# Kernel optimization log

Hardware: AMD Instinct MI355X
Metric: run time of the kernel (lower is better)

## Reference

```python
import jax, jax.numpy as jnp
import numpy as np

B = 8192          # batch
DEPTH = 2         # variational layers
NCLS = 10         # classes
WIRES = 4         # qubits -> 16-dim statevector
NPATCH = 196      # 14x14 patches of 2x2 on a 28x28 image

# Pauli-Z expectation table: row i = (+1/-1) per wire for basis state i (wire 0 = MSB)
_bits = (np.arange(16)[:, None] >> np.array([3, 2, 1, 0])) & 1
_ZTAB = jnp.asarray(1.0 - 2.0 * _bits, dtype=jnp.float32)  # (16, 4)


def _ry(state, ang, wire):
    # Apply RY(ang) (real rotation) on `wire`; state shape (N,2,2,2,2)
    c = jnp.cos(0.5 * ang)
    s = jnp.sin(0.5 * ang)
    a0 = jnp.take(state, 0, axis=wire + 1)
    a1 = jnp.take(state, 1, axis=wire + 1)
    return jnp.stack([c * a0 - s * a1, s * a0 + c * a1], axis=wire + 1)


def _cnot01(state):  # control wire 0 (axis 1), target wire 1 (axis 2)
    return jnp.stack([state[:, 0], state[:, 1, ::-1]], axis=1)


def _cnot23(state):  # control wire 2 (axis 3), target wire 3 (axis 4)
    return jnp.stack([state[:, :, :, 0], state[:, :, :, 1, ::-1]], axis=3)


def _quanv(patches, theta):
    # patches: (N, 4) pixel angles. Batched 4-qubit statevector simulation.
    half = 0.5 * patches
    v = jnp.stack([jnp.cos(half), jnp.sin(half)], axis=-1)  # (N,4,2): RY(x_w)|0>
    state = jnp.einsum('na,nb,nc,nd->nabcd', v[:, 0], v[:, 1], v[:, 2], v[:, 3])
    for d in range(theta.shape[0]):
        for w in range(WIRES):
            state = _ry(state, theta[d, w], w)
        state = _cnot01(state)
        state = _cnot23(state)
    probs = (state * state).reshape(state.shape[0], 16)
    return probs @ _ZTAB  # (N, 4) <Z_w> expectations


def setup_inputs() -> dict:
    key = jax.random.key(0)
    k1, k2, k3 = jax.random.split(key, 3)
    x = jax.random.normal(k1, (B, 1, 28, 28), dtype=jnp.float32)
    theta = jax.random.normal(k2, (DEPTH, WIRES), dtype=jnp.float32)
    W = jax.random.normal(k3, (NCLS, NPATCH * WIRES), dtype=jnp.float32) * 0.03
    b = jnp.zeros((NCLS,), dtype=jnp.float32)
    return {"x": x, "theta": theta, "W": W, "b": b}


def reference(x, theta, W, b):
    bsz = x.shape[0]
    # extract 2x2 patches in (row-block, col-block) order, pixels row-major
    patches = (x[:, 0]
               .reshape(bsz, 14, 2, 14, 2)
               .transpose(0, 1, 3, 2, 4)
               .reshape(bsz * NPATCH, 4))
    qfeat = _quanv(patches, theta).reshape(bsz, NPATCH * WIRES)  # (B, 784)
    logits = qfeat @ W.T + b
    return jax.nn.log_softmax(logits, axis=-1)
```

## Files before the change

kernel.cpp:

```cpp
#include <hip/hip_runtime.h>
#include <math.h>

#define NP 196
#define NC 10

__device__ __forceinline__ void sim_pair(float pxa, float pxb,
                                         float th0a, float th0b,
                                         float ct0, float st0,
                                         float ct1, float st1,
                                         float& z0, float& z1) {
    float sa, ca, sb, cb;
    __sincosf(0.5f * (pxa + th0a), &sa, &ca);
    __sincosf(0.5f * (pxb + th0b), &sb, &cb);
    float p0 = ca * cb, p1 = ca * sb, p2 = sa * sb, p3 = sa * cb;
    float q0 = ct0 * p0 - st0 * p2, q2 = st0 * p0 + ct0 * p2;
    float q1 = ct0 * p1 - st0 * p3, q3 = st0 * p1 + ct0 * p3;
    float r0 = ct1 * q0 - st1 * q1, r1 = st1 * q0 + ct1 * q1;
    float r2 = ct1 * q2 - st1 * q3, r3 = st1 * q2 + ct1 * q3;
    float e0 = r0 * r0, e1 = r1 * r1, e2 = r2 * r2, e3 = r3 * r3;
    z0 = (e0 + e1) - (e2 + e3);
    z1 = (e0 - e1) + (e3 - e2);
}

__global__ __launch_bounds__(256) void quanv_fused(
    const float* __restrict__ x,
    const float* __restrict__ theta,
    const float* __restrict__ W,
    const float* __restrict__ bias,
    float* __restrict__ out,
    int B)
{
    __shared__ float s_th0[4], s_ct1[4], s_st1[4], s_bias[NC];
    const int tid = threadIdx.x;
    if (tid < 4) {
        s_th0[tid] = theta[tid];
        float sv, cv;
        __sincosf(0.5f * theta[4 + tid], &sv, &cv);
        s_st1[tid] = sv;
        s_ct1[tid] = cv;
    }
    if (tid < NC) s_bias[tid] = bias[tid];
    __syncthreads();

    const int lane = tid & 63;
    const int wave = blockIdx.x * 4 + (tid >> 6);
    const int imgA = wave * 2;
    if (imgA >= B) return;

    const float th00 = s_th0[0], th01 = s_th0[1], th02 = s_th0[2], th03 = s_th0[3];
    const float ctA0 = s_ct1[0], stA0 = s_st1[0], ctA1 = s_ct1[1], stA1 = s_st1[1];
    const float ctB0 = s_ct1[2], stB0 = s_st1[2], ctB1 = s_ct1[3], stB1 = s_st1[3];

    const float* xA = x + (size_t)imgA * 784;
    const float* xB = xA + 784;

    float accA[NC], accB[NC];
#pragma unroll
    for (int c = 0; c < NC; ++c) { accA[c] = 0.f; accB[c] = 0.f; }

#pragma unroll
    for (int k = 0; k < 4; ++k) {
        const int p = lane + 64 * k;
        if (k == 3 && p >= NP) break;
        const int i = p / 14;
        const int j = p - i * 14;
        const int off = i * 56 + j * 2;

        const float2 a0 = *(const float2*)(xA + off);
        const float2 a1 = *(const float2*)(xA + off + 28);
        const float2 b0 = *(const float2*)(xB + off);
        const float2 b1 = *(const float2*)(xB + off + 28);

        float fA[4], fB[4];
        sim_pair(a0.x, a0.y, th00, th01, ctA0, stA0, ctA1, stA1, fA[0], fA[1]);
        sim_pair(a1.x, a1.y, th02, th03, ctB0, stB0, ctB1, stB1, fA[2], fA[3]);
        sim_pair(b0.x, b0.y, th00, th01, ctA0, stA0, ctA1, stA1, fB[0], fB[1]);
        sim_pair(b1.x, b1.y, th02, th03, ctB0, stB0, ctB1, stB1, fB[2], fB[3]);

#pragma unroll
        for (int c = 0; c < NC; ++c) {
            const float4 w4 = *(const float4*)(W + c * 784 + p * 4);
            accA[c] = fmaf(fA[0], w4.x, fmaf(fA[1], w4.y,
                      fmaf(fA[2], w4.z, fmaf(fA[3], w4.w, accA[c]))));
            accB[c] = fmaf(fB[0], w4.x, fmaf(fB[1], w4.y,
                      fmaf(fB[2], w4.z, fmaf(fB[3], w4.w, accB[c]))));
        }
    }

#pragma unroll
    for (int c = 0; c < NC; ++c) {
        float vA = accA[c], vB = accB[c];
#pragma unroll
        for (int m = 1; m < 64; m <<= 1) {
            vA += __shfl_xor(vA, m);
            vB += __shfl_xor(vB, m);
        }
        accA[c] = vA + s_bias[c];
        accB[c] = vB + s_bias[c];
    }

    float lg[NC];
#pragma unroll
    for (int c = 0; c < NC; ++c) lg[c] = (lane < 32) ? accA[c] : accB[c];

    float m = lg[0];
#pragma unroll
    for (int c = 1; c < NC; ++c) m = fmaxf(m, lg[c]);
    float se = 0.f;
#pragma unroll
    for (int c = 0; c < NC; ++c) se += __expf(lg[c] - m);
    const float lse = m + __logf(se);

    const int wl = lane & 31;
    const int img = imgA + (lane >> 5);
    if (wl < NC) out[img * NC + wl] = lg[wl] - lse;
}

extern "C" void kernel_launch(void* const* d_in, const int* in_sizes, int n_in,
                              void* d_out, int out_size, void* d_ws, size_t ws_size,
                              hipStream_t stream) {
    const float* x     = (const float*)d_in[0];
    const float* theta = (const float*)d_in[1];
    const float* W     = (const float*)d_in[2];
    const float* bias  = (const float*)d_in[3];
    float* out = (float*)d_out;
    const int B = in_sizes[0] / 784;
    const int waves = (B + 1) / 2;
    const int blocks = (waves + 3) / 4;
    quanv_fused<<<blocks, 256, 0, stream>>>(x, theta, W, bias, out, B);
}
```

Measured before the change: 17.03 us.

## Process four images per wave and use DPP/swizzle transpose-reduction

```diff
diff --git a/kernel.cpp b/kernel.cpp
--- a/kernel.cpp
+++ b/kernel.cpp
@@ -3,6 +3,18 @@
 
 #define NP 196
 #define NC 10
+
+
+template<int CTRL>
+__device__ __forceinline__ float dpp_add(float v) {
+    int t = __builtin_amdgcn_update_dpp(0, __float_as_int(v), CTRL, 0xF, 0xF, true);
+    return v + __int_as_float(t);
+}
+
+__device__ __forceinline__ float swz_xor16_add(float v) {
+    int t = __builtin_amdgcn_ds_swizzle(__float_as_int(v), 0x401F);
+    return v + __int_as_float(t);
+}
 
 __device__ __forceinline__ void sim_pair(float pxa, float pxb,
                                          float th0a, float th0b,
@@ -22,7 +34,7 @@
     z1 = (e0 - e1) + (e3 - e2);
 }
 
-__global__ __launch_bounds__(256) void quanv_fused(
+__global__ __launch_bounds__(256, 2) void quanv_fused(
     const float* __restrict__ x,
     const float* __restrict__ theta,
     const float* __restrict__ W,
@@ -30,90 +42,93 @@
     float* __restrict__ out,
     int B)
 {
-    __shared__ float s_th0[4], s_ct1[4], s_st1[4], s_bias[NC];
-    const int tid = threadIdx.x;
-    if (tid < 4) {
-        s_th0[tid] = theta[tid];
-        float sv, cv;
-        __sincosf(0.5f * theta[4 + tid], &sv, &cv);
-        s_st1[tid] = sv;
-        s_ct1[tid] = cv;
-    }
-    if (tid < NC) s_bias[tid] = bias[tid];
-    __syncthreads();
-
+    const int tid  = threadIdx.x;
     const int lane = tid & 63;
     const int wave = blockIdx.x * 4 + (tid >> 6);
-    const int imgA = wave * 2;
-    if (imgA >= B) return;
+    const int imgbase = wave * 4;
+    if (imgbase >= B) return;
 
-    const float th00 = s_th0[0], th01 = s_th0[1], th02 = s_th0[2], th03 = s_th0[3];
-    const float ctA0 = s_ct1[0], stA0 = s_st1[0], ctA1 = s_ct1[1], stA1 = s_st1[1];
-    const float ctB0 = s_ct1[2], stB0 = s_st1[2], ctB1 = s_ct1[3], stB1 = s_st1[3];
+    const float th00 = theta[0], th01 = theta[1], th02 = theta[2], th03 = theta[3];
+    float ct[4], st[4];
+#pragma unroll
+    for (int w = 0; w < 4; ++w) __sincosf(0.5f * theta[4 + w], &st[w], &ct[w]);
 
-    const float* xA = x + (size_t)imgA * 784;
-    const float* xB = xA + 784;
+    const float* x0 = x + (size_t)imgbase * 784;
 
-    float accA[NC], accB[NC];
+    float acc[4][NC];
 #pragma unroll
-    for (int c = 0; c < NC; ++c) { accA[c] = 0.f; accB[c] = 0.f; }
+    for (int m = 0; m < 4; ++m)
+#pragma unroll
+        for (int c = 0; c < NC; ++c) acc[m][c] = 0.f;
 
 #pragma unroll
     for (int k = 0; k < 4; ++k) {
+        const bool active = (k < 3) || (lane < 4);
         const int p = lane + 64 * k;
-        if (k == 3 && p >= NP) break;
-        const int i = p / 14;
-        const int j = p - i * 14;
-        const int off = i * 56 + j * 2;
+        const int pi = p / 14;
+        const int pj = p - pi * 14;
+        const int off = pi * 56 + pj * 2;
 
-        const float2 a0 = *(const float2*)(xA + off);
-        const float2 a1 = *(const float2*)(xA + off + 28);
-        const float2 b0 = *(const float2*)(xB + off);
-        const float2 b1 = *(const float2*)(xB + off + 28);
-
-        float fA[4], fB[4];
-        sim_pair(a0.x, a0.y, th00, th01, ctA0, stA0, ctA1, stA1, fA[0], fA[1]);
-        sim_pair(a1.x, a1.y, th02, th03, ctB0, stB0, ctB1, stB1, fA[2], fA[3]);
-        sim_pair(b0.x, b0.y, th00, th01, ctA0, stA0, ctA1, stA1, fB[0], fB[1]);
-        sim_pair(b1.x, b1.y, th02, th03, ctB0, stB0, ctB1, stB1, fB[2], fB[3]);
-
+        float f[4][4];
+        if (active) {
 #pragma unroll
-        for (int c = 0; c < NC; ++c) {
-            const float4 w4 = *(const float4*)(W + c * 784 + p * 4);
-            accA[c] = fmaf(fA[0], w4.x, fmaf(fA[1], w4.y,
-                      fmaf(fA[2], w4.z, fmaf(fA[3], w4.w, accA[c]))));
-            accB[c] = fmaf(fB[0], w4.x, fmaf(fB[1], w4.y,
-                      fmaf(fB[2], w4.z, fmaf(fB[3], w4.w, accB[c]))));
+            for (int m = 0; m < 4; ++m) {
+                const float* xm = x0 + m * 784 + off;
+                const float2 r0 = *(const float2*)(xm);
+                const float2 r1 = *(const float2*)(xm + 28);
+                sim_pair(r0.x, r0.y, th00, th01, ct[0], st[0], ct[1], st[1],
+                         f[m][0], f[m][1]);
+                sim_pair(r1.x, r1.y, th02, th03, ct[2], st[2], ct[3], st[3],
+                         f[m][2], f[m][3]);
+            }
+#pragma unroll
+            for (int c = 0; c < NC; ++c) {
+                const float4 w4 = *(const float4*)(W + c * 784 + p * 4);
+#pragma unroll
+                for (int m = 0; m < 4; ++m) {
+                    acc[m][c] = fmaf(f[m][0], w4.x, fmaf(f[m][1], w4.y,
+                                fmaf(f[m][2], w4.z, fmaf(f[m][3], w4.w, acc[m][c]))));
+                }
+            }
         }
     }
 
+    const bool lo32 = (lane & 32) == 0;
+    const bool lo16 = (lane & 16) == 0;
+    float m4[NC];
 #pragma unroll
     for (int c = 0; c < NC; ++c) {
-        float vA = accA[c], vB = accB[c];
-#pragma unroll
-        for (int m = 1; m < 64; m <<= 1) {
-            vA += __shfl_xor(vA, m);
-            vB += __shfl_xor(vB, m);
-        }
-        accA[c] = vA + s_bias[c];
-        accB[c] = vB + s_bias[c];
+        float tAB = lo32 ? acc[0][c] : acc[1][c];
+        float uAB = lo32 ? acc[1][c] : acc[0][c];
+        float mAB = tAB + __shfl_xor(uAB, 32);
+        float tCD = lo32 ? acc[2][c] : acc[3][c];
+        float uCD = lo32 ? acc[3][c] : acc[2][c];
+        float mCD = tCD + __shfl_xor(uCD, 32);
+        float t = lo16 ? mAB : mCD;
+        float u = lo16 ? mCD : mAB;
+        float v = t + swz_xor16_add(u) - u;
+        v = dpp_add<0x124>(v);
+        v = dpp_add<0x128>(v);
+        v = dpp_add<0xB1>(v);
+        v = dpp_add<0x4E>(v);
+        m4[c] = v + bias[c];
     }
 
-    float lg[NC];
+    float mx = m4[0];
 #pragma unroll
-    for (int c = 0; c < NC; ++c) lg[c] = (lane < 32) ? accA[c] : accB[c];
-
-    float m = lg[0];
-#pragma unroll
-    for (int c = 1; c < NC; ++c) m = fmaxf(m, lg[c]);
+    for (int c = 1; c < NC; ++c) mx = fmaxf(mx, m4[c]);
     float se = 0.f;
 #pragma unroll
-    for (int c = 0; c < NC; ++c) se += __expf(lg[c] - m);
-    const float lse = m + __logf(se);
+    for (int c = 0; c < NC; ++c) se += __expf(m4[c] - mx);
+    const float lse = mx + __logf(se);
 
-    const int wl = lane & 31;
-    const int img = imgA + (lane >> 5);
-    if (wl < NC) out[img * NC + wl] = lg[wl] - lse;
+    const int r  = lane >> 4;
+    const int cl = lane & 15;
+    const int img = imgbase + ((r & 1) << 1) + (r >> 1);
+    float val = m4[0];
+#pragma unroll
+    for (int c = 1; c < NC; ++c) val = (cl == c) ? m4[c] : val;
+    if (cl < NC) out[img * NC + cl] = val - lse;
 }
 
 extern "C" void kernel_launch(void* const* d_in, const int* in_sizes, int n_in,
@@ -125,7 +140,7 @@
     const float* bias  = (const float*)d_in[3];
     float* out = (float*)d_out;
     const int B = in_sizes[0] / 784;
-    const int waves = (B + 1) / 2;
+    const int waves  = (B + 3) / 4;
     const int blocks = (waves + 3) / 4;
     quanv_fused<<<blocks, 256, 0, stream>>>(x, theta, W, bias, out, B);
 }
```

Result: faster. 15.64 us (median of 2 runs) (-8.2%).
